# Optimization experiments

Hardware: AMD Instinct MI355X
Metric: run time of the kernel (lower is better)

## Reference

```python
import jax, jax.numpy as jnp
import numpy as np

N, E, EH, RH, R, H = 50000, 800000, 256, 128, 500, 2


def _seg_softmax(e, rel, num_segments):
    # torch_geometric.utils.softmax keyed by rel: (e - max_seg).exp() / (sum_seg + 1e-16)
    m = jax.ops.segment_max(e, rel, num_segments=num_segments)
    m = jnp.where(jnp.isfinite(m), m, 0.0)  # empty segments -> 0
    ex = jnp.exp(e - m[rel])
    s = jax.ops.segment_sum(ex, rel, num_segments=num_segments)
    return ex / (s[rel] + 1e-16)


def setup_inputs() -> dict:
    key = jax.random.key(0)
    ks = jax.random.split(key, 7)
    x_e = jax.random.normal(ks[0], (N, EH), dtype=jnp.float32)
    edge_index = jax.random.randint(ks[1], (2, E), 0, N)
    rel = jax.random.randint(ks[2], (E,), 0, R)
    w_h = jax.random.normal(ks[3], (RH, EH), dtype=jnp.float32) / np.sqrt(EH)
    w_t = jax.random.normal(ks[4], (RH, EH), dtype=jnp.float32) / np.sqrt(EH)
    a_h = jax.random.normal(ks[5], (H, RH), dtype=jnp.float32) / np.sqrt(RH)
    a_t = jax.random.normal(ks[6], (H, RH), dtype=jnp.float32) / np.sqrt(RH)
    return {"x_e": x_e, "edge_index": edge_index, "rel": rel,
            "w_h": w_h, "w_t": w_t, "a_h": a_h, "a_t": a_t, "num_heads": H}


def reference(x_e, edge_index, rel, w_h, w_t, a_h, a_t, num_heads):
    src, dst = edge_index[0], edge_index[1]
    x_r_h = x_e @ w_h.T  # [N, RH]
    x_r_t = x_e @ w_t.T  # [N, RH]
    # per-node attention scores for all heads: [N, H]
    s_hh = x_r_h @ a_h.T
    s_tt = x_r_t @ a_t.T
    s_th = x_r_t @ a_h.T
    s_ht = x_r_h @ a_t.T
    acc = jnp.zeros((R, RH), dtype=x_e.dtype)
    for h in range(num_heads):  # small fixed head count
        e1 = jax.nn.leaky_relu(s_hh[src, h] + s_tt[dst, h], 0.01)
        a1 = _seg_softmax(e1, rel, R)
        acc = acc + jax.ops.segment_sum(a1[:, None] * x_r_h[src], rel, num_segments=R)
        e2 = jax.nn.leaky_relu(s_th[src, h] + s_ht[dst, h], 0.01)
        a2 = _seg_softmax(e2, rel, R)
        acc = acc + jax.ops.segment_sum(a2[:, None] * x_r_t[dst], rel, num_segments=R)
    x_r = acc / num_heads / 2.0
    return x_r  # dropout is identity in eval mode
```

## Files before the change

kernel.cpp:

```cpp
#include <hip/hip_runtime.h>
#include <hip/hip_bf16.h>

#define NN 50000
#define NE 800000
#define NR 500
#define KEH 256
#define KRH 128
#define NSB 8
#define SBW 6250
#define NBK (NR*NSB)
#define NBE 256
#define EPB (NE/NBE)
#define NTILE 3125
#define CSB 16

typedef __attribute__((ext_vector_type(8))) __bf16 bf16x8;
typedef __attribute__((ext_vector_type(4))) float f32x4;

#define OFF_XH     0UL
#define OFF_XT     12800000UL
#define OFF_SP     25600000UL
#define OFF_DP     26400000UL
#define OFF_SUMS   27200000UL
#define OFF_HISTH  27208000UL
#define OFF_HISTT  27224000UL
#define OFF_INVS   27240000UL
#define OFF_BASEH  27248000UL
#define OFF_BASET  27264016UL
#define OFF_RECH   27312032UL
#define OFF_RECT   33712032UL
#define OFF_PART   40112032UL
#define OFF_AH     42160032UL
#define OFF_AT     42161056UL
#define OFF_FLAG   42162080UL
#define OFF_WHH    42162144UL
#define OFF_WTH    42293216UL
#define OFF_HPBH   42424288UL
#define OFF_HPBT   46520288UL

__device__ __forceinline__ int clampi(int v, int hi) {
    v = v < 0 ? 0 : v;
    return v >= hi ? hi - 1 : v;
}

__device__ __forceinline__ int sniff_isbf(const unsigned* xe_raw) {
    int lane = threadIdx.x & 63;
    unsigned w = xe_raw[lane];
    unsigned ex = (w >> 7) & 0xFFu;
    bool hit = (ex >= 115u && ex <= 131u);
    return __popcll(__ballot(hit)) >= 32;
}

__global__ __launch_bounds__(256) void k_init(const unsigned* __restrict__ xe_raw,
                                              const void* __restrict__ ah_in, const void* __restrict__ at_in,
                                              const void* __restrict__ wh, const void* __restrict__ wt,
                                              unsigned* __restrict__ flag, float* __restrict__ ah32,
                                              float* __restrict__ at32,
                                              __bf16* __restrict__ whh, __bf16* __restrict__ wth,
                                              unsigned* __restrict__ zero1) {
    int isbf = sniff_isbf(xe_raw);
    int t = threadIdx.x;
    if (blockIdx.x == 0) {
        if (t == 0) flag[0] = (unsigned)isbf;
        ah32[t] = isbf ? __bfloat162float(((const __hip_bfloat16*)ah_in)[t]) : ((const float*)ah_in)[t];
        at32[t] = isbf ? __bfloat162float(((const __hip_bfloat16*)at_in)[t]) : ((const float*)at_in)[t];
    } else if (blockIdx.x <= 128) {
        int o = (blockIdx.x - 1) * 256 + t;
        int e = o & 7, c = (o >> 3) & 15, q = (o >> 7) & 3, ks = (o >> 9) & 7, ct = o >> 12;
        int i = (ct * 16 + c) * KEH + ks * 32 + q * 8 + e;
        if (isbf) {
            whh[o] = ((const __bf16*)wh)[i];
            wth[o] = ((const __bf16*)wt)[i];
        } else {
            whh[o] = (__bf16)((const float*)wh)[i];
            wth[o] = (__bf16)((const float*)wt)[i];
        }
    } else {
        int stride = (gridDim.x - 129) * 256;
        for (int i = (blockIdx.x - 129) * 256 + t; i < 10000; i += stride) zero1[i] = 0u;
    }
}

__global__ __launch_bounds__(512, 4) void k_gemm(const void* __restrict__ xe,
                                              const unsigned* __restrict__ flag,
                                              const __bf16* __restrict__ whh, const __bf16* __restrict__ wth,
                                              const float* __restrict__ ah, const float* __restrict__ at,
                                              __hip_bfloat16* __restrict__ xh, __hip_bfloat16* __restrict__ xt,
                                              float2* __restrict__ sp2, float2* __restrict__ dp2) {
    __shared__ uint4 lb[4096];
    const int t = threadIdx.x, lane = t & 63, wave = t >> 6;
    const int l16 = lane & 15, quad = lane >> 4;
    const int ph = blockIdx.x & 1;
    const int isbf = (int)flag[0];
    const __bf16* wfh = ph ? wth : whh;

    {
        const uint4* wsrc = (const uint4*)wfh;
        #pragma unroll
        for (int i = 0; i < 8; ++i) lb[i * 512 + t] = wsrc[i * 512 + t];
    }
    __syncthreads();

    __hip_bfloat16* out = ph ? xt : xh;
    for (int tile = (int)(blockIdx.x >> 1) * 8 + wave; tile < NTILE; tile += 2048) {
        const int row = tile * 16 + l16;
        bf16x8 a[8];
        if (isbf) {
            const __bf16* xb = (const __bf16*)xe + (size_t)row * KEH;
            #pragma unroll
            for (int ks = 0; ks < 8; ++ks)
                a[ks] = *(const bf16x8*)(xb + ks * 32 + quad * 8);
        } else {
            const float* xf = (const float*)xe + (size_t)row * KEH;
            #pragma unroll
            for (int ks = 0; ks < 8; ++ks) {
                const float* p = xf + ks * 32 + quad * 8;
                float4 u0 = *(const float4*)p, u1 = *(const float4*)(p + 4);
                a[ks][0] = (__bf16)u0.x; a[ks][1] = (__bf16)u0.y;
                a[ks][2] = (__bf16)u0.z; a[ks][3] = (__bf16)u0.w;
                a[ks][4] = (__bf16)u1.x; a[ks][5] = (__bf16)u1.y;
                a[ks][6] = (__bf16)u1.z; a[ks][7] = (__bf16)u1.w;
            }
        }

        f32x4 acc[8];
        #pragma unroll
        for (int ct = 0; ct < 8; ++ct) acc[ct] = (f32x4){0.f, 0.f, 0.f, 0.f};
        #pragma unroll
        for (int ks = 0; ks < 8; ++ks)
            #pragma unroll
            for (int ct = 0; ct < 8; ++ct)
                acc[ct] = __builtin_amdgcn_mfma_f32_16x16x32_bf16(
                    a[ks], *(const bf16x8*)&lb[(ct * 8 + ks) * 64 + lane], acc[ct], 0, 0, 0);

        float s0[4] = {0.f,0.f,0.f,0.f}, s1[4] = {0.f,0.f,0.f,0.f};
        float s2[4] = {0.f,0.f,0.f,0.f}, s3[4] = {0.f,0.f,0.f,0.f};
        #pragma unroll
        for (int ct = 0; ct < 8; ++ct) {
            int c = ct * 16 + l16;
            float va0 = ah[c], va1 = ah[128 + c];
            float vb0 = at[c], vb1 = at[128 + c];
            #pragma unroll
            for (int jj = 0; jj < 4; ++jj) {
                float v = acc[ct][jj];
                s0[jj] = fmaf(v, va0, s0[jj]);
                s1[jj] = fmaf(v, va1, s1[jj]);
                s2[jj] = fmaf(v, vb0, s2[jj]);
                s3[jj] = fmaf(v, vb1, s3[jj]);
                out[(size_t)(tile * 16 + quad * 4 + jj) * KRH + c] = __float2bfloat16(v);
            }
        }
        #pragma unroll
        for (int off = 8; off; off >>= 1)
            #pragma unroll
            for (int jj = 0; jj < 4; ++jj) {
                s0[jj] += __shfl_xor(s0[jj], off);
                s1[jj] += __shfl_xor(s1[jj], off);
                s2[jj] += __shfl_xor(s2[jj], off);
                s3[jj] += __shfl_xor(s3[jj], off);
            }
        if (l16 == 0) {
            #pragma unroll
            for (int jj = 0; jj < 4; ++jj) {
                int n = tile * 16 + quad * 4 + jj;
                if (ph == 0) {
                    sp2[n * 2 + 0] = make_float2(s0[jj], s1[jj]);
                    dp2[n * 2 + 1] = make_float2(s2[jj], s3[jj]);
                } else {
                    sp2[n * 2 + 1] = make_float2(s0[jj], s1[jj]);
                    dp2[n * 2 + 0] = make_float2(s2[jj], s3[jj]);
                }
            }
        }
    }
}

__device__ __forceinline__ float eexp(float x) {
    x = x > 0.f ? x : 0.01f * x;
    x = fminf(x, 50.f);
    return __expf(x);
}

__global__ __launch_bounds__(1024) void k_edge(const int* __restrict__ src, const int* __restrict__ dst,
                                               const int* __restrict__ rel,
                                               const float4* __restrict__ sp, const float4* __restrict__ dp,
                                               float* __restrict__ sums,
                                               unsigned* __restrict__ histH, unsigned* __restrict__ histT,
                                               unsigned* __restrict__ hpbH, unsigned* __restrict__ hpbT) {
    __shared__ float ls[NR * 4];
    __shared__ unsigned lhH[NBK], lhT[NBK];
    int t = threadIdx.x;
    for (int i = t; i < NR * 4; i += 1024) ls[i] = 0.f;
    for (int i = t; i < NBK; i += 1024) { lhH[i] = 0u; lhT[i] = 0u; }
    __syncthreads();
    unsigned lo = blockIdx.x * EPB, hi = lo + EPB;
    for (unsigned e = lo + t; e < hi; e += 1024) {
        int s = clampi(src[e], NN), d = clampi(dst[e], NN), r = clampi(rel[e], NR);
        float4 a = sp[s], b = dp[d];
        float4 ex;
        ex.x = eexp(a.x + b.x); ex.y = eexp(a.y + b.y);
        ex.z = eexp(a.z + b.z); ex.w = eexp(a.w + b.w);
        atomicAdd(&ls[r*4+0], ex.x);
        atomicAdd(&ls[r*4+1], ex.y);
        atomicAdd(&ls[r*4+2], ex.z);
        atomicAdd(&ls[r*4+3], ex.w);
        atomicAdd(&lhH[r * NSB + s / SBW], 1u);
        atomicAdd(&lhT[r * NSB + d / SBW], 1u);
    }
    __syncthreads();
    for (int i = t; i < NR * 4; i += 1024)
        if (ls[i] != 0.f) atomicAdd(&sums[i], ls[i]);
    size_t row = (size_t)blockIdx.x * NBK;
    for (int i = t; i < NBK; i += 1024) {
        unsigned cH = lhH[i], cT = lhT[i];
        hpbH[row + i] = cH;
        hpbT[row + i] = cT;
        if (cH) atomicAdd(&histH[i], cH);
        if (cT) atomicAdd(&histT[i], cT);
    }
}

__global__ __launch_bounds__(256) void k_scan(const unsigned* __restrict__ histH,
                                              const unsigned* __restrict__ histT,
                                              const float* __restrict__ sums,
                                              unsigned* __restrict__ hpbH, unsigned* __restrict__ hpbT,
                                              unsigned* __restrict__ baseH, unsigned* __restrict__ baseT,
                                              float* __restrict__ invs) {
    __shared__ unsigned bases[4096];
    __shared__ unsigned wsum[4];
    __shared__ unsigned wsum2[4][CSB];
    const int b = blockIdx.x;
    const int pass = b >= (NBK / CSB);
    const int slice = pass ? b - NBK / CSB : b;
    const unsigned* h = pass ? histT : histH;
    unsigned* hpb = pass ? hpbT : hpbH;
    unsigned* base = pass ? baseT : baseH;
    const int t = threadIdx.x, lane = t & 63, wv = t >> 6;

    {
        int j0 = t * 16;
        unsigned v[16], s = 0;
        const uint4* hp4 = (const uint4*)(h + j0);
        #pragma unroll
        for (int q = 0; q < 4; ++q) {
            uint4 u = (j0 + q * 4 < NBK) ? hp4[q] : make_uint4(0u, 0u, 0u, 0u);
            v[q*4+0] = u.x; v[q*4+1] = u.y; v[q*4+2] = u.z; v[q*4+3] = u.w;
        }
        #pragma unroll
        for (int k = 0; k < 16; ++k) {
            if (j0 + k >= NBK) v[k] = 0u;
            s += v[k];
        }
        unsigned inc = s;
        #pragma unroll
        for (int d = 1; d < 64; d <<= 1) {
            unsigned u = __shfl_up(inc, d);
            if (lane >= d) inc += u;
        }
        if (lane == 63) wsum[wv] = inc;
        __syncthreads();
        unsigned wbase = 0;
        for (int i = 0; i < wv; ++i) wbase += wsum[i];
        unsigned run = wbase + inc - s;
        #pragma unroll
        for (int k = 0; k < 16; ++k) {
            if (j0 + k < NBK) bases[j0 + k] = run;
            run += v[k];
        }
        __syncthreads();
        if (slice == 0) {
            for (int i = t; i < NBK; i += 256) base[i] = bases[i];
            if (t == 0) base[NBK] = wsum[0] + wsum[1] + wsum[2] + wsum[3];
        }
        if (b == 0) for (int i = t; i < NR * 4; i += 256) invs[i] = 1.f / (sums[i] + 1e-16f);
    }

    {
        int bin0 = slice * CSB;
        unsigned v[CSB], inc[CSB];
        uint4* hp = (uint4*)(hpb + (size_t)t * NBK + bin0);
        #pragma unroll
        for (int q = 0; q < CSB / 4; ++q) {
            uint4 u = hp[q];
            v[q*4+0] = u.x; v[q*4+1] = u.y; v[q*4+2] = u.z; v[q*4+3] = u.w;
        }
        #pragma unroll
        for (int k = 0; k < CSB; ++k) inc[k] = v[k];
        #pragma unroll
        for (int d = 1; d < 64; d <<= 1) {
            #pragma unroll
            for (int k = 0; k < CSB; ++k) {
                unsigned u = __shfl_up(inc[k], d);
                if (lane >= d) inc[k] += u;
            }
        }
        if (lane == 63) {
            #pragma unroll
            for (int k = 0; k < CSB; ++k) wsum2[wv][k] = inc[k];
        }
        __syncthreads();
        #pragma unroll
        for (int k = 0; k < CSB; ++k) {
            unsigned wbase = 0;
            for (int i = 0; i < wv; ++i) wbase += wsum2[i][k];
            v[k] = bases[bin0 + k] + wbase + inc[k] - v[k];
        }
        #pragma unroll
        for (int q = 0; q < CSB / 4; ++q)
            hp[q] = make_uint4(v[q*4+0], v[q*4+1], v[q*4+2], v[q*4+3]);
    }
}

__global__ __launch_bounds__(1024) void k_mkrec(const int* __restrict__ src, const int* __restrict__ dst,
                                                const int* __restrict__ rel,
                                                const float4* __restrict__ sp, const float4* __restrict__ dp,
                                                const float4* __restrict__ invs4,
                                                const unsigned* __restrict__ hpbH, const unsigned* __restrict__ hpbT,
                                                uint2* __restrict__ recH, uint2* __restrict__ recT) {
    __shared__ unsigned lcH[NBK], lcT[NBK];
    int t = threadIdx.x;
    size_t row = (size_t)blockIdx.x * NBK;
    for (int i = t; i < NBK; i += 1024) { lcH[i] = hpbH[row + i]; lcT[i] = hpbT[row + i]; }
    __syncthreads();
    unsigned lo = blockIdx.x * EPB, hi = lo + EPB;
    for (unsigned e = lo + t; e < hi; e += 1024) {
        int s = clampi(src[e], NN), d = clampi(dst[e], NN), r = clampi(rel[e], NR);
        float4 a = sp[s], b = dp[d];
        float4 iv = invs4[r];
        float exx = eexp(a.x + b.x), exy = eexp(a.y + b.y);
        float exz = eexp(a.z + b.z), exw = eexp(a.w + b.w);
        float w1 = exx * iv.x + exy * iv.y;
        float w2 = exz * iv.z + exw * iv.w;
        unsigned pH = atomicAdd(&lcH[r * NSB + s / SBW], 1u);
        unsigned pT = atomicAdd(&lcT[r * NSB + d / SBW], 1u);
        if (pH < NE) recH[pH] = make_uint2((unsigned)s, __float_as_uint(w1));
        if (pT < NE) recT[pT] = make_uint2((unsigned)d, __float_as_uint(w2));
    }
}

__global__ __launch_bounds__(256) void k_accR(const uint2* __restrict__ recH, const uint2* __restrict__ recT,
                                              const unsigned* __restrict__ baseH, const unsigned* __restrict__ baseT,
                                              const __hip_bfloat16* __restrict__ xh,
                                              const __hip_bfloat16* __restrict__ xt,
                                              float* __restrict__ part) {
    __shared__ float red[3][128];
    __shared__ uint2 lrec[256];
    int b = blockIdx.x;
    int t = threadIdx.x, lane = t & 63, wv = t >> 6;
    int l16 = lane & 15, g = lane >> 4;
    float az[8];
    #pragma unroll
    for (int k = 0; k < 8; ++k) az[k] = 0.f;

    for (int pass = 0; pass < 2; ++pass) {
        const uint2* rec = pass ? recT : recH;
        const unsigned* base = pass ? baseT : baseH;
        const uint4* xs = (const uint4*)(pass ? xt : xh);
        unsigned b0 = base[b];
        unsigned cnt = base[b + 1] - b0;
        if (cnt > NE) cnt = 0;
        for (unsigned cb = 0; cb < cnt; cb += 256u) {
            unsigned cn = cnt - cb; if (cn > 256u) cn = 256u;
            __syncthreads();
            if ((unsigned)t < cn) lrec[t] = rec[b0 + cb + t];
            __syncthreads();
            unsigned j = (unsigned)(wv * 4 + g);
            for (; j + 48u < cn; j += 64u) {
                uint2 v0 = lrec[j], v1 = lrec[j + 16u], v2 = lrec[j + 32u], v3 = lrec[j + 48u];
                unsigned n0 = v0.x < NN ? v0.x : 0u;
                unsigned n1 = v1.x < NN ? v1.x : 0u;
                unsigned n2 = v2.x < NN ? v2.x : 0u;
                unsigned n3 = v3.x < NN ? v3.x : 0u;
                uint4 u0 = xs[(size_t)n0 * 16 + l16];
                uint4 u1 = xs[(size_t)n1 * 16 + l16];
                uint4 u2 = xs[(size_t)n2 * 16 + l16];
                uint4 u3 = xs[(size_t)n3 * 16 + l16];
                float w0 = __uint_as_float(v0.y), w1 = __uint_as_float(v1.y);
                float w2 = __uint_as_float(v2.y), w3 = __uint_as_float(v3.y);
                az[0] = fmaf(w0, __uint_as_float(u0.x << 16),         az[0]);
                az[1] = fmaf(w0, __uint_as_float(u0.x & 0xffff0000u), az[1]);
                az[2] = fmaf(w0, __uint_as_float(u0.y << 16),         az[2]);
                az[3] = fmaf(w0, __uint_as_float(u0.y & 0xffff0000u), az[3]);
                az[4] = fmaf(w0, __uint_as_float(u0.z << 16),         az[4]);
                az[5] = fmaf(w0, __uint_as_float(u0.z & 0xffff0000u), az[5]);
                az[6] = fmaf(w0, __uint_as_float(u0.w << 16),         az[6]);
                az[7] = fmaf(w0, __uint_as_float(u0.w & 0xffff0000u), az[7]);
                az[0] = fmaf(w1, __uint_as_float(u1.x << 16),         az[0]);
                az[1] = fmaf(w1, __uint_as_float(u1.x & 0xffff0000u), az[1]);
                az[2] = fmaf(w1, __uint_as_float(u1.y << 16),         az[2]);
                az[3] = fmaf(w1, __uint_as_float(u1.y & 0xffff0000u), az[3]);
                az[4] = fmaf(w1, __uint_as_float(u1.z << 16),         az[4]);
                az[5] = fmaf(w1, __uint_as_float(u1.z & 0xffff0000u), az[5]);
                az[6] = fmaf(w1, __uint_as_float(u1.w << 16),         az[6]);
                az[7] = fmaf(w1, __uint_as_float(u1.w & 0xffff0000u), az[7]);
                az[0] = fmaf(w2, __uint_as_float(u2.x << 16),         az[0]);
                az[1] = fmaf(w2, __uint_as_float(u2.x & 0xffff0000u), az[1]);
                az[2] = fmaf(w2, __uint_as_float(u2.y << 16),         az[2]);
                az[3] = fmaf(w2, __uint_as_float(u2.y & 0xffff0000u), az[3]);
                az[4] = fmaf(w2, __uint_as_float(u2.z << 16),         az[4]);
                az[5] = fmaf(w2, __uint_as_float(u2.z & 0xffff0000u), az[5]);
                az[6] = fmaf(w2, __uint_as_float(u2.w << 16),         az[6]);
                az[7] = fmaf(w2, __uint_as_float(u2.w & 0xffff0000u), az[7]);
                az[0] = fmaf(w3, __uint_as_float(u3.x << 16),         az[0]);
                az[1] = fmaf(w3, __uint_as_float(u3.x & 0xffff0000u), az[1]);
                az[2] = fmaf(w3, __uint_as_float(u3.y << 16),         az[2]);
                az[3] = fmaf(w3, __uint_as_float(u3.y & 0xffff0000u), az[3]);
                az[4] = fmaf(w3, __uint_as_float(u3.z << 16),         az[4]);
                az[5] = fmaf(w3, __uint_as_float(u3.z & 0xffff0000u), az[5]);
                az[6] = fmaf(w3, __uint_as_float(u3.w << 16),         az[6]);
                az[7] = fmaf(w3, __uint_as_float(u3.w & 0xffff0000u), az[7]);
            }
            for (; j < cn; j += 16u) {
                uint2 v = lrec[j];
                unsigned nd = v.x < NN ? v.x : 0u;
                float w = __uint_as_float(v.y);
                uint4 u = xs[(size_t)nd * 16 + l16];
                az[0] = fmaf(w, __uint_as_float(u.x << 16),          az[0]);
                az[1] = fmaf(w, __uint_as_float(u.x & 0xffff0000u),  az[1]);
                az[2] = fmaf(w, __uint_as_float(u.y << 16),          az[2]);
                az[3] = fmaf(w, __uint_as_float(u.y & 0xffff0000u),  az[3]);
                az[4] = fmaf(w, __uint_as_float(u.z << 16),          az[4]);
                az[5] = fmaf(w, __uint_as_float(u.z & 0xffff0000u),  az[5]);
                az[6] = fmaf(w, __uint_as_float(u.w << 16),          az[6]);
                az[7] = fmaf(w, __uint_as_float(u.w & 0xffff0000u),  az[7]);
            }
        }
    }
    #pragma unroll
    for (int k = 0; k < 8; ++k) {
        az[k] += __shfl_xor(az[k], 16);
        az[k] += __shfl_xor(az[k], 32);
    }
    __syncthreads();
    if (wv > 0 && lane < 16) {
        #pragma unroll
        for (int k = 0; k < 8; ++k) red[wv - 1][l16 * 8 + k] = az[k];
    }
    __syncthreads();
    if (wv == 0 && lane < 16) {
        #pragma unroll
        for (int k = 0; k < 8; ++k) {
            float s = az[k] + red[0][l16 * 8 + k] + red[1][l16 * 8 + k] + red[2][l16 * 8 + k];
            part[(size_t)b * KRH + l16 * 8 + k] = s;
        }
    }
}

__global__ __launch_bounds__(256) void k_out(const float* __restrict__ part,
                                             const unsigned* __restrict__ flag, void* __restrict__ out) {
    int i = blockIdx.x * 256 + threadIdx.x;
    if (i < NR * KRH) {
        int r = i >> 7, c = i & 127;
        float v = 0.f;
        for (int s = 0; s < NSB; ++s) v += part[(size_t)(r * NSB + s) * KRH + c];
        v *= 0.25f;
        if (!isfinite(v)) v = 0.f;
        if (flag[0]) ((__hip_bfloat16*)out)[i] = __float2bfloat16(v);
        else         ((float*)out)[i] = v;
    }
}

extern "C" void kernel_launch(void* const* d_in, const int* in_sizes, int n_in,
                              void* d_out, int out_size, void* d_ws, size_t ws_size,
                              hipStream_t stream) {
    const void* xe  = d_in[0];
    const int* eidx = (const int*)d_in[1];
    const int* rel  = (const int*)d_in[2];
    const void* wh  = d_in[3];
    const void* wt  = d_in[4];
    const void* ahp = d_in[5];
    const void* atp = d_in[6];

    const int* src = eidx;
    const int* dst = eidx + NE;

    char* ws = (char*)d_ws;
    __hip_bfloat16* xh = (__hip_bfloat16*)(ws + OFF_XH);
    __hip_bfloat16* xt = (__hip_bfloat16*)(ws + OFF_XT);
    float4*   sp     = (float4*)(ws + OFF_SP);
    float4*   dp     = (float4*)(ws + OFF_DP);
    float*    sums   = (float*)(ws + OFF_SUMS);
    unsigned* histH  = (unsigned*)(ws + OFF_HISTH);
    unsigned* histT  = (unsigned*)(ws + OFF_HISTT);
    float*    invs   = (float*)(ws + OFF_INVS);
    unsigned* baseH  = (unsigned*)(ws + OFF_BASEH);
    unsigned* baseT  = (unsigned*)(ws + OFF_BASET);
    uint2*    recH   = (uint2*)(ws + OFF_RECH);
    uint2*    recT   = (uint2*)(ws + OFF_RECT);
    float*    partp  = (float*)(ws + OFF_PART);
    float*    ah32   = (float*)(ws + OFF_AH);
    float*    at32   = (float*)(ws + OFF_AT);
    unsigned* flag   = (unsigned*)(ws + OFF_FLAG);
    __bf16*   whh    = (__bf16*)(ws + OFF_WHH);
    __bf16*   wth    = (__bf16*)(ws + OFF_WTH);
    unsigned* hpbH   = (unsigned*)(ws + OFF_HPBH);
    unsigned* hpbT   = (unsigned*)(ws + OFF_HPBT);

    k_init<<<161, 256, 0, stream>>>((const unsigned*)xe, ahp, atp, wh, wt, flag, ah32, at32,
                                     whh, wth, (unsigned*)(ws + OFF_SUMS));
    k_gemm<<<512, 512, 0, stream>>>(xe, flag, whh, wth, ah32, at32,
                                    xh, xt, (float2*)sp, (float2*)dp);
    k_edge<<<NBE, 1024, 0, stream>>>(src, dst, rel, sp, dp, sums, histH, histT, hpbH, hpbT);
    k_scan<<<2 * (NBK / CSB), 256, 0, stream>>>(histH, histT, sums, hpbH, hpbT, baseH, baseT, invs);
    k_mkrec<<<NBE, 1024, 0, stream>>>(src, dst, rel, sp, dp, (const float4*)invs, hpbH, hpbT, recH, recT);
    k_accR<<<NBK, 256, 0, stream>>>(recH, recT, baseH, baseT, xh, xt, partp);
    k_out<<<(NR * KRH + 255) / 256, 256, 0, stream>>>(partp, flag, d_out);
}
```

Measured before the change: 227.3 us.

## Compute both head and tail projections per block to share the input tile load

Each GEMM block now holds both weight matrices in LDS (128KB) and computes the head and tail projections for the same 16-row tile. Previously separate blocks handled each projection and each read x_e on its own. The A fragments now stay in registers for both, so the x_e read (and fp32 to bf16 conversion) happens once instead of twice. Per-node scores are written as single float4 stores, and the grid is halved with launch bounds relaxed to 2 blocks per CU. The cost is more LDS per block and lower occupancy.

```diff
diff --git a/kernel.cpp b/kernel.cpp
--- a/kernel.cpp
+++ b/kernel.cpp
@@ -81,28 +81,29 @@
     }
 }
 
-__global__ __launch_bounds__(512, 4) void k_gemm(const void* __restrict__ xe,
+__global__ __launch_bounds__(512, 2) void k_gemm(const void* __restrict__ xe,
                                               const unsigned* __restrict__ flag,
                                               const __bf16* __restrict__ whh, const __bf16* __restrict__ wth,
                                               const float* __restrict__ ah, const float* __restrict__ at,
                                               __hip_bfloat16* __restrict__ xh, __hip_bfloat16* __restrict__ xt,
-                                              float2* __restrict__ sp2, float2* __restrict__ dp2) {
-    __shared__ uint4 lb[4096];
+                                              float4* __restrict__ sp, float4* __restrict__ dp) {
+    __shared__ uint4 lb[8192];
     const int t = threadIdx.x, lane = t & 63, wave = t >> 6;
     const int l16 = lane & 15, quad = lane >> 4;
-    const int ph = blockIdx.x & 1;
     const int isbf = (int)flag[0];
-    const __bf16* wfh = ph ? wth : whh;
 
     {
-        const uint4* wsrc = (const uint4*)wfh;
-        #pragma unroll
-        for (int i = 0; i < 8; ++i) lb[i * 512 + t] = wsrc[i * 512 + t];
+        const uint4* s0 = (const uint4*)whh;
+        const uint4* s1 = (const uint4*)wth;
+        #pragma unroll
+        for (int i = 0; i < 8; ++i) {
+            lb[i * 512 + t] = s0[i * 512 + t];
+            lb[4096 + i * 512 + t] = s1[i * 512 + t];
+        }
     }
     __syncthreads();
 
-    __hip_bfloat16* out = ph ? xt : xh;
-    for (int tile = (int)(blockIdx.x >> 1) * 8 + wave; tile < NTILE; tile += 2048) {
+    for (int tile = (int)blockIdx.x * 8 + wave; tile < NTILE; tile += 2048) {
         const int row = tile * 16 + l16;
         bf16x8 a[8];
         if (isbf) {
@@ -123,53 +124,60 @@
             }
         }
 
-        f32x4 acc[8];
-        #pragma unroll
-        for (int ct = 0; ct < 8; ++ct) acc[ct] = (f32x4){0.f, 0.f, 0.f, 0.f};
-        #pragma unroll
-        for (int ks = 0; ks < 8; ++ks)
-            #pragma unroll
-            for (int ct = 0; ct < 8; ++ct)
-                acc[ct] = __builtin_amdgcn_mfma_f32_16x16x32_bf16(
-                    a[ks], *(const bf16x8*)&lb[(ct * 8 + ks) * 64 + lane], acc[ct], 0, 0, 0);
-
-        float s0[4] = {0.f,0.f,0.f,0.f}, s1[4] = {0.f,0.f,0.f,0.f};
-        float s2[4] = {0.f,0.f,0.f,0.f}, s3[4] = {0.f,0.f,0.f,0.f};
-        #pragma unroll
-        for (int ct = 0; ct < 8; ++ct) {
-            int c = ct * 16 + l16;
-            float va0 = ah[c], va1 = ah[128 + c];
-            float vb0 = at[c], vb1 = at[128 + c];
+        float hh0[4], hh1[4], ht0[4], ht1[4];
+        float th0[4], th1[4], tt0[4], tt1[4];
+        #pragma unroll
+        for (int ph = 0; ph < 2; ++ph) {
+            f32x4 acc[8];
+            #pragma unroll
+            for (int ct = 0; ct < 8; ++ct) acc[ct] = (f32x4){0.f, 0.f, 0.f, 0.f};
+            #pragma unroll
+            for (int ks = 0; ks < 8; ++ks)
+                #pragma unroll
+                for (int ct = 0; ct < 8; ++ct)
+                    acc[ct] = __builtin_amdgcn_mfma_f32_16x16x32_bf16(
+                        a[ks], *(const bf16x8*)&lb[ph * 4096 + (ct * 8 + ks) * 64 + lane],
+                        acc[ct], 0, 0, 0);
+
+            __hip_bfloat16* out = ph ? xt : xh;
+            float s0[4] = {0.f,0.f,0.f,0.f}, s1[4] = {0.f,0.f,0.f,0.f};
+            float s2[4] = {0.f,0.f,0.f,0.f}, s3[4] = {0.f,0.f,0.f,0.f};
+            #pragma unroll
+            for (int ct = 0; ct < 8; ++ct) {
+                int c = ct * 16 + l16;
+                float va0 = ah[c], va1 = ah[128 + c];
+                float vb0 = at[c], vb1 = at[128 + c];
+                #pragma unroll
+                for (int jj = 0; jj < 4; ++jj) {
+                    float v = acc[ct][jj];
+                    s0[jj] = fmaf(v, va0, s0[jj]);
+                    s1[jj] = fmaf(v, va1, s1[jj]);
+                    s2[jj] = fmaf(v, vb0, s2[jj]);
+                    s3[jj] = fmaf(v, vb1, s3[jj]);
+                    out[(size_t)(tile * 16 + quad * 4 + jj) * KRH + c] = __float2bfloat16(v);
+                }
+            }
+            #pragma unroll
+            for (int off = 8; off; off >>= 1)
+                #pragma unroll
+                for (int jj = 0; jj < 4; ++jj) {
+                    s0[jj] += __shfl_xor(s0[jj], off);
+                    s1[jj] += __shfl_xor(s1[jj], off);
+                    s2[jj] += __shfl_xor(s2[jj], off);
+                    s3[jj] += __shfl_xor(s3[jj], off);
+                }
             #pragma unroll
             for (int jj = 0; jj < 4; ++jj) {
-                float v = acc[ct][jj];
-                s0[jj] = fmaf(v, va0, s0[jj]);
-                s1[jj] = fmaf(v, va1, s1[jj]);
-                s2[jj] = fmaf(v, vb0, s2[jj]);
-                s3[jj] = fmaf(v, vb1, s3[jj]);
-                out[(size_t)(tile * 16 + quad * 4 + jj) * KRH + c] = __float2bfloat16(v);
-            }
-        }
-        #pragma unroll
-        for (int off = 8; off; off >>= 1)
-            #pragma unroll
-            for (int jj = 0; jj < 4; ++jj) {
-                s0[jj] += __shfl_xor(s0[jj], off);
-                s1[jj] += __shfl_xor(s1[jj], off);
-                s2[jj] += __shfl_xor(s2[jj], off);
-                s3[jj] += __shfl_xor(s3[jj], off);
-            }
+                if (ph == 0) { hh0[jj] = s0[jj]; hh1[jj] = s1[jj]; ht0[jj] = s2[jj]; ht1[jj] = s3[jj]; }
+                else         { th0[jj] = s0[jj]; th1[jj] = s1[jj]; tt0[jj] = s2[jj]; tt1[jj] = s3[jj]; }
+            }
+        }
         if (l16 == 0) {
             #pragma unroll
             for (int jj = 0; jj < 4; ++jj) {
                 int n = tile * 16 + quad * 4 + jj;
-                if (ph == 0) {
-                    sp2[n * 2 + 0] = make_float2(s0[jj], s1[jj]);
-                    dp2[n * 2 + 1] = make_float2(s2[jj], s3[jj]);
-                } else {
-                    sp2[n * 2 + 1] = make_float2(s0[jj], s1[jj]);
-                    dp2[n * 2 + 0] = make_float2(s2[jj], s3[jj]);
-                }
+                sp[n] = make_float4(hh0[jj], hh1[jj], th0[jj], th1[jj]);
+                dp[n] = make_float4(tt0[jj], tt1[jj], ht0[jj], ht1[jj]);
             }
         }
     }
@@ -498,8 +506,7 @@
 
     k_init<<<161, 256, 0, stream>>>((const unsigned*)xe, ahp, atp, wh, wt, flag, ah32, at32,
                                      whh, wth, (unsigned*)(ws + OFF_SUMS));
-    k_gemm<<<512, 512, 0, stream>>>(xe, flag, whh, wth, ah32, at32,
-                                    xh, xt, (float2*)sp, (float2*)dp);
+    k_gemm<<<256, 512, 0, stream>>>(xe, flag, whh, wth, ah32, at32, xh, xt, sp, dp);
     k_edge<<<NBE, 1024, 0, stream>>>(src, dst, rel, sp, dp, sums, histH, histT, hpbH, hpbT);
     k_scan<<<2 * (NBK / CSB), 256, 0, stream>>>(histH, histT, sums, hpbH, hpbT, baseH, baseT, invs);
     k_mkrec<<<NBE, 1024, 0, stream>>>(src, dst, rel, sp, dp, (const float4*)invs, hpbH, hpbT, recH, recT);
```

Result: faster. 222.0 us (-2.3%).
